# Optimization experiments

Measured on AMD Instinct MI355X. Metric: run time of the kernel, lower is better.

Reference implementation:

```python
import jax, jax.numpy as jnp
import numpy as np

EMBED = 512
HEADS = 8
HEAD_DIM = EMBED // HEADS
WINDOW = 256
HALF = WINDOW // 2
B, S = 2, 2048


def setup_inputs() -> dict:
    key = jax.random.key(0)
    kv, kk, kq, kw = jax.random.split(key, 4)
    return {
        "values": jax.random.normal(kv, (B, 1, S, EMBED), dtype=jnp.float32),
        "keys": jax.random.normal(kk, (B, 1, S, EMBED), dtype=jnp.float32),
        "query": jax.random.normal(kq, (B, 1, S, EMBED), dtype=jnp.float32),
        "mask": jnp.ones((B, 1, 1, S), dtype=jnp.int32),
        "fc_w": jax.random.normal(kw, (EMBED, EMBED), dtype=jnp.float32) * (1.0 / np.sqrt(EMBED)),
        "fc_b": jnp.zeros((EMBED,), dtype=jnp.float32),
    }


def reference(values, keys, query, mask, fc_w, fc_b):
    b = query.shape[0]
    s = values.shape[2]
    v = values.reshape(b, s, HEADS, HEAD_DIM)
    k = keys.reshape(b, s, HEADS, HEAD_DIM)
    q = query.reshape(b, s, HEADS, HEAD_DIM)
    scale = jnp.float32(EMBED ** 0.5)

    # global token: query 0 attends to all keys
    gq = q[:, 0:1]  # (b,1,h,d)
    ge = jnp.einsum('bqhd,bkhd->bhqk', gq, k)
    ga = jax.nn.softmax(ge / scale, axis=3)
    gout = jnp.einsum('bhqk,bkhd->bqhd', ga, v)  # (b,1,h,d)

    # sliding-window queries (positions 1..s-1, band centered at local index i)
    wq = q[:, 1:]  # (b, s-1, h, d)
    qw = s - 1
    e = jnp.einsum('bqhd,bkhd->bhqk', wq, k)  # (b,h,qw,s)
    i = jnp.arange(qw)[:, None]
    j = jnp.arange(s)[None, :]
    band = (j >= i - HALF) & (j <= i + HALF)  # (qw, s)
    # faithful to original: out-of-band energies are ZERO (not -inf)
    e = jnp.where(band[None, None], e, jnp.float32(0.0))
    e = jnp.where(mask == 0, jnp.float32(-1e20), e)
    a = jax.nn.softmax(e / scale, axis=3)
    lout = jnp.einsum('bhqk,bkhd->bqhd', a, v)  # (b,qw,h,d)

    out = jnp.concatenate([gout, lout], axis=1).reshape(b, s, HEADS * HEAD_DIM)
    return out @ fc_w.T + fc_b
```

## Files before the change

kernel.cpp:

```cpp
#include <hip/hip_runtime.h>
#include <math.h>

#define EMBED 512
#define HEADS 8
#define HDIM 64
#define SLEN 2048
#define BATCH 2
#define HALFW 128
#define NCHUNK 32
#define INV_SCALE 0.044194173824159216f

typedef short bf16x8 __attribute__((ext_vector_type(8)));
typedef short s16x4  __attribute__((ext_vector_type(4)));
typedef float f32x4  __attribute__((ext_vector_type(4)));

#define MFMA16(a, b, c) __builtin_amdgcn_mfma_f32_16x16x32_bf16(a, b, c, 0, 0, 0)

__device__ __forceinline__ short f2bf(float x) {
    union { float f; unsigned u; } v; v.f = x;
    unsigned r = v.u + 0x7FFFu + ((v.u >> 16) & 1u);
    return (short)(r >> 16);
}

__device__ __forceinline__ int lidx(int row, int seg) {
    return (((seg << 6) + (row ^ seg)) << 3);
}

__device__ __forceinline__ void gll16(const short* g, short* l) {
    __builtin_amdgcn_global_load_lds(
        (const __attribute__((address_space(1))) unsigned int*)g,
        (__attribute__((address_space(3))) unsigned int*)l, 16, 0, 0);
}

__device__ __forceinline__ void stage_chunk(const short* s0, const short* s1,
                                            short* d0, short* d1, int t) {
    int off = t * 8;
    int wb  = (t >> 6) * 512;
    gll16(s0 + off,        d0 + wb);
    gll16(s0 + 2048 + off, d0 + 2048 + wb);
    gll16(s1 + off,        d1 + wb);
    gll16(s1 + 2048 + off, d1 + 2048 + wb);
}

__device__ __forceinline__ void stage_tile(const short* s, short* d, int t) {
    int off = t * 8;
    int wb  = (t >> 6) * 512;
    gll16(s + off,        d + wb);
    gll16(s + 2048 + off, d + 2048 + wb);
}

__global__ __launch_bounds__(256) void prepass(
    const float* __restrict__ q, const float* __restrict__ k,
    const float* __restrict__ v, const int* __restrict__ mask,
    const float* __restrict__ fcw,
    short* __restrict__ Kbf, short* __restrict__ Vbf, short* __restrict__ Wbf,
    float* __restrict__ gnum_part, float* __restrict__ gden_part,
    float* __restrict__ vsum_part, float* __restrict__ nval_part) {
    int d = blockIdx.x;
    int x = d & 7, i = d >> 3;
    int hb8 = x * 2 + (i >= 68);
    int ii  = (i >= 68) ? (i - 68) : i;
    int h = hb8 & 7, b = hb8 >> 3;
    int t = threadIdx.x, w = t >> 6, l = t & 63;

    if (ii >= 64) {
        int widx = hb8 * 4 + (ii - 64);
        int nb = widx >> 3, kt = widx & 7;
        size_t base = (size_t)(nb * 8 + kt) * 4096;
        #pragma unroll
        for (int p = 0; p < 4; ++p) {
            int idx = p * 256 + t, row = idx >> 4, kg = idx & 15;
            float4 f = *(const float4*)(fcw + (size_t)(nb * 64 + row) * EMBED + kt * 64 + kg * 4);
            s16x4 o;
            o[0] = f2bf(f.x); o[1] = f2bf(f.y); o[2] = f2bf(f.z); o[3] = f2bf(f.w);
            *(s16x4*)&Wbf[base + lidx(row, kg >> 1) + (kg & 1) * 4] = o;
        }
        return;
    }

    int ch  = ii;
    int c   = ch >> 1;
    int rof = (ch & 1) * 32;
    int j0  = ch * 32;

    __shared__ float q0s[HDIM];
    __shared__ float wls[32];
    __shared__ int   m_s[32];
    __shared__ float vbuf[32][68];
    __shared__ float red[4][HDIM];
    __shared__ float redv[4][HDIM];

    if (t < 64) q0s[t] = q[(size_t)b * SLEN * EMBED + h * HDIM + t];
    else if (t < 96) m_s[t - 64] = mask[b * SLEN + j0 + (t - 64)];
    __syncthreads();

    size_t fragbase = ((size_t)(b * HEADS + h) * NCHUNK + c) * 4096;

    #pragma unroll
    for (int p = 0; p < 2; ++p) {
        int idx = p * 256 + t, row = idx >> 4, kg = idx & 15;
        float4 f = *(const float4*)(k + ((size_t)b * SLEN + j0 + row) * EMBED + h * HDIM + kg * 4);
        float dot = q0s[kg*4+0]*f.x + q0s[kg*4+1]*f.y + q0s[kg*4+2]*f.z + q0s[kg*4+3]*f.w;
        dot += __shfl_xor(dot, 1, 64);
        dot += __shfl_xor(dot, 2, 64);
        dot += __shfl_xor(dot, 4, 64);
        dot += __shfl_xor(dot, 8, 64);
        if ((t & 15) == 0) wls[row] = __expf(dot * INV_SCALE);
        if (!m_s[row]) f = make_float4(0.f, 0.f, 0.f, 0.f);
        s16x4 o;
        o[0] = f2bf(f.x); o[1] = f2bf(f.y); o[2] = f2bf(f.z); o[3] = f2bf(f.w);
        *(s16x4*)&Kbf[fragbase + lidx(rof + row, kg >> 1) + (kg & 1) * 4] = o;
    }

    #pragma unroll
    for (int p = 0; p < 2; ++p) {
        int idx = p * 256 + t, row = idx >> 4, kg = idx & 15;
        float4 f = *(const float4*)(v + ((size_t)b * SLEN + j0 + row) * EMBED + h * HDIM + kg * 4);
        *(float4*)&vbuf[row][kg * 4] = f;
    }
    __syncthreads();

    float num = 0.f, vs = 0.f;
    #pragma unroll
    for (int jj = 0; jj < 8; ++jj) {
        int jl = w * 8 + jj;
        float vv = vbuf[jl][l];
        num += wls[jl] * vv;
        if (m_s[jl]) vs += vv;
    }
    red[w][l] = num;
    redv[w][l] = vs;

    {
        int jseg = (ch & 1) * 4 + w;
        bf16x8 o;
        #pragma unroll
        for (int e = 0; e < 8; ++e) o[e] = f2bf(vbuf[w * 8 + e][l]);
        *(bf16x8*)&Vbf[fragbase + lidx(l, jseg)] = o;
    }
    __syncthreads();

    if (w == 0) {
        gnum_part[((size_t)(b * HEADS + h) * 64 + ch) * HDIM + l] =
            red[0][l] + red[1][l] + red[2][l] + red[3][l];
        vsum_part[((size_t)b * 64 + ch) * EMBED + h * HDIM + l] =
            redv[0][l] + redv[1][l] + redv[2][l] + redv[3][l];
    } else if (w == 1) {
        float s = (l < 32) ? wls[l] : 0.f;
        #pragma unroll
        for (int off = 32; off > 0; off >>= 1) s += __shfl_xor(s, off, 64);
        if (l == 0) gden_part[(size_t)(b * HEADS + h) * 64 + ch] = s;
    } else if (w == 2 && h == 0) {
        float cc = (l < 32 && m_s[l]) ? 1.f : 0.f;
        #pragma unroll
        for (int off = 32; off > 0; off >>= 1) cc += __shfl_xor(cc, off, 64);
        if (l == 0) nval_part[b * 64 + ch] = cc;
    }
}

__global__ __launch_bounds__(256) void windowed_attn_v9(
    const float* __restrict__ q, const float* __restrict__ k,
    const float* __restrict__ v, const int* __restrict__ mask,
    const short* __restrict__ Kbf, const short* __restrict__ Vbf,
    const float* __restrict__ gnum_part, const float* __restrict__ gden_part,
    const float* __restrict__ vsum_part, const float* __restrict__ nval_part,
    short* __restrict__ Abf) {
    int dsp = blockIdx.x;
    int wid = (dsp & 7) * 64 + (dsp >> 3);
    int tile = wid & 31, h = (wid >> 5) & 7, b = wid >> 8;
    int r0 = tile * 64;
    int t = threadIdx.x, w = t >> 6, l = t & 63;
    int lg = l >> 4, lr = l & 15;

    __shared__ __align__(16) short k_s[4][4096];
    __shared__ __align__(16) short v_s[4][4096];
    __shared__ __align__(16) short wT_s[4][16][72];
    __shared__ float rsum[64];
    __shared__ float vred[4][64];
    __shared__ float gred[4][64];
    __shared__ float nv_s, gd_s;

    size_t hb = (size_t)(b * HEADS + h) * NCHUNK;
    int bh = b * HEADS + h;

    int c0 = tile - 2; if (c0 < 0) c0 = 0;
    int c1 = tile + 2; if (c1 > NCHUNK - 1) c1 = NCHUNK - 1;

    stage_chunk(Kbf + (hb + c0) * 4096, Vbf + (hb + c0) * 4096,
                &k_s[0][0], &v_s[0][0], t);

    const float* qrow = q + ((size_t)b * SLEN + r0 + w * 16 + lr) * EMBED + h * HDIM;
    float4 a0 = *(const float4*)(qrow + lg * 8);
    float4 a1 = *(const float4*)(qrow + lg * 8 + 4);
    float4 a2 = *(const float4*)(qrow + 32 + lg * 8);
    float4 a3 = *(const float4*)(qrow + 32 + lg * 8 + 4);
    bf16x8 qb0, qb1;
    qb0[0] = f2bf(a0.x); qb0[1] = f2bf(a0.y); qb0[2] = f2bf(a0.z); qb0[3] = f2bf(a0.w);
    qb0[4] = f2bf(a1.x); qb0[5] = f2bf(a1.y); qb0[6] = f2bf(a1.z); qb0[7] = f2bf(a1.w);
    qb1[0] = f2bf(a2.x); qb1[1] = f2bf(a2.y); qb1[2] = f2bf(a2.z); qb1[3] = f2bf(a2.w);
    qb1[4] = f2bf(a3.x); qb1[5] = f2bf(a3.y); qb1[6] = f2bf(a3.z); qb1[7] = f2bf(a3.w);

    {
        float vp = 0.f;
        #pragma unroll
        for (int cc = 0; cc < 16; ++cc)
            vp += vsum_part[((size_t)b * 64 + w * 16 + cc) * EMBED + h * HDIM + l];
        vred[w][l] = vp;
        if (w == 0) {
            float nvv = nval_part[b * 64 + l];
            #pragma unroll
            for (int off = 32; off > 0; off >>= 1) nvv += __shfl_xor(nvv, off, 64);
            if (l == 0) nv_s = nvv;
        }
        if (tile == 0) {
            float gp = 0.f;
            #pragma unroll
            for (int cc = 0; cc < 16; ++cc)
                gp += gnum_part[((size_t)bh * 64 + w * 16 + cc) * HDIM + l];
            gred[w][l] = gp;
            if (w == 1) {
                float gdd = gden_part[(size_t)bh * 64 + l];
                #pragma unroll
                for (int off = 32; off > 0; off >>= 1) gdd += __shfl_xor(gdd, off, 64);
                if (l == 0) gd_s = gdd;
            }
        }
    }

    stage_chunk(Kbf + (hb + c0 + 1) * 4096, Vbf + (hb + c0 + 1) * 4096,
                &k_s[1][0], &v_s[1][0], t);
    stage_chunk(Kbf + (hb + c0 + 2) * 4096, Vbf + (hb + c0 + 2) * 4096,
                &k_s[2][0], &v_s[2][0], t);

    int center = r0 + w * 16 + lr - 1;
    int lo = center - HALFW, hi = center + HALFW;

    f32x4 pv[4];
    #pragma unroll
    for (int dt = 0; dt < 4; ++dt) pv[dt] = (f32x4){0.f, 0.f, 0.f, 0.f};
    float dacc = 0.f;

    int bi = 0;
    for (int c = c0; c <= c1; ++c) {
        int rem = c1 - c;
        if (rem >= 2)      { asm volatile("s_waitcnt vmcnt(8)" ::: "memory"); }
        else if (rem == 1) { asm volatile("s_waitcnt vmcnt(4)" ::: "memory"); }
        else               { asm volatile("s_waitcnt vmcnt(0)" ::: "memory"); }
        __syncthreads();

        int jc = c * 64;
        #pragma unroll
        for (int jt = 0; jt < 4; ++jt) {
            bf16x8 ka0 = *(const bf16x8*)&k_s[bi][lidx(jt * 16 + lr, lg)];
            bf16x8 ka1 = *(const bf16x8*)&k_s[bi][lidx(jt * 16 + lr, 4 + lg)];
            f32x4 sT = (f32x4){0.f, 0.f, 0.f, 0.f};
            sT = MFMA16(ka0, qb0, sT);
            sT = MFMA16(ka1, qb1, sT);
            int jbase = jc + jt * 16 + lg * 4;
            s16x4 wq;
            #pragma unroll
            for (int r = 0; r < 4; ++r) {
                int j = jbase + r;
                float wgt = (j >= lo && j <= hi) ? (__expf(sT[r] * INV_SCALE) - 1.f) : 0.f;
                dacc += wgt;
                wq[r] = f2bf(wgt);
            }
            *(s16x4*)&wT_s[w][lr][jt * 16 + lg * 4] = wq;
        }

        bf16x8 wa0 = *(const bf16x8*)&wT_s[w][lr][lg * 8];
        bf16x8 wa1 = *(const bf16x8*)&wT_s[w][lr][32 + lg * 8];
        #pragma unroll
        for (int dt = 0; dt < 4; ++dt) {
            bf16x8 va0 = *(const bf16x8*)&v_s[bi][lidx(dt * 16 + lr, lg)];
            bf16x8 va1 = *(const bf16x8*)&v_s[bi][lidx(dt * 16 + lr, 4 + lg)];
            pv[dt] = MFMA16(wa0, va0, pv[dt]);
            pv[dt] = MFMA16(wa1, va1, pv[dt]);
        }

        if (c + 3 <= c1) {
            int bn = (bi + 3) & 3;
            stage_chunk(Kbf + (hb + c + 3) * 4096, Vbf + (hb + c + 3) * 4096,
                        &k_s[bn][0], &v_s[bn][0], t);
        }
        bi = (bi + 1) & 3;
    }

    float wfix = 0.f;
    int jx = r0 - 129;
    if (w == 0 && jx >= 0) {
        float qv = q[((size_t)b * SLEN + r0) * EMBED + h * HDIM + l];
        float kv = k[((size_t)b * SLEN + jx) * EMBED + h * HDIM + l];
        float dd = qv * kv;
        #pragma unroll
        for (int off = 32; off > 0; off >>= 1) dd += __shfl_xor(dd, off, 64);
        if (mask[b * SLEN + jx] != 0) wfix = __expf(dd * INV_SCALE) - 1.f;
        if (lg == 0) {
            #pragma unroll
            for (int dt = 0; dt < 4; ++dt)
                pv[dt][0] += wfix * v[((size_t)b * SLEN + jx) * EMBED + h * HDIM + dt * 16 + lr];
        }
    }

    dacc += __shfl_xor(dacc, 16, 64);
    dacc += __shfl_xor(dacc, 32, 64);
    if (lg == 0) rsum[w * 16 + lr] = dacc + ((w == 0 && lr == 0) ? wfix : 0.f);
    __syncthreads();

    float nv = nv_s;
    float invden[4];
    #pragma unroll
    for (int r = 0; r < 4; ++r)
        invden[r] = 1.f / (nv + rsum[w * 16 + lg * 4 + r]);

    short* Atile = Abf + ((size_t)(b * NCHUNK + tile) * 8 + h) * 4096;
    #pragma unroll
    for (int dt = 0; dt < 4; ++dt) {
        int d = dt * 16 + lr;
        float vs = vred[0][d] + vred[1][d] + vred[2][d] + vred[3][d];
        #pragma unroll
        for (int r = 0; r < 4; ++r) {
            int row_local = w * 16 + lg * 4 + r;
            float o;
            if (tile == 0 && row_local == 0)
                o = (gred[0][d] + gred[1][d] + gred[2][d] + gred[3][d]) / gd_s;
            else
                o = (pv[dt][r] + vs) * invden[r];
            Atile[lidx(row_local, d >> 3) + (d & 7)] = f2bf(o);
        }
    }
}

__global__ __launch_bounds__(256) void fc_gemm_v5(
    const short* __restrict__ Abf, const short* __restrict__ Wbf,
    const float* __restrict__ bias, float* __restrict__ C) {
    int bm = blockIdx.x;
    int nb = blockIdx.y;
    int t = threadIdx.x, w = t >> 6, l = t & 63;
    int lg = l >> 4, lr = l & 15;
    int wr = w >> 1, wc = w & 1;

    __shared__ __align__(16) short a_s[8][4096];
    __shared__ __align__(16) short w_s[2][4096];

    stage_tile(Abf + (size_t)(bm * 8 + 0) * 4096, &a_s[0][0], t);
    stage_tile(Wbf + (size_t)(nb * 8 + 0) * 4096, &w_s[0][0], t);
    stage_tile(Wbf + (size_t)(nb * 8 + 1) * 4096, &w_s[1][0], t);
    #pragma unroll
    for (int kt = 1; kt < 8; ++kt)
        stage_tile(Abf + (size_t)(bm * 8 + kt) * 4096, &a_s[kt][0], t);

    f32x4 acc[2][2];
    #pragma unroll
    for (int mt = 0; mt < 2; ++mt)
        #pragma unroll
        for (int nt = 0; nt < 2; ++nt) acc[mt][nt] = (f32x4){0.f, 0.f, 0.f, 0.f};

    for (int kt = 0; kt < 8; ++kt) {
        if (kt == 0)      { asm volatile("s_waitcnt vmcnt(16)" ::: "memory"); }
        else if (kt == 1) { asm volatile("s_waitcnt vmcnt(14)" ::: "memory"); }
        else if (kt < 7)  { asm volatile("s_waitcnt vmcnt(2)"  ::: "memory"); }
        else              { asm volatile("s_waitcnt vmcnt(0)"  ::: "memory"); }
        __syncthreads();

        bf16x8 af[2][2], bf_[2][2];
        #pragma unroll
        for (int mt = 0; mt < 2; ++mt) {
            af[mt][0] = *(const bf16x8*)&a_s[kt][lidx(wr * 32 + mt * 16 + lr, lg)];
            af[mt][1] = *(const bf16x8*)&a_s[kt][lidx(wr * 32 + mt * 16 + lr, 4 + lg)];
        }
        int wbuf = kt & 1;
        #pragma unroll
        for (int nt = 0; nt < 2; ++nt) {
            bf_[nt][0] = *(const bf16x8*)&w_s[wbuf][lidx(wc * 32 + nt * 16 + lr, lg)];
            bf_[nt][1] = *(const bf16x8*)&w_s[wbuf][lidx(wc * 32 + nt * 16 + lr, 4 + lg)];
        }
        #pragma unroll
        for (int mt = 0; mt < 2; ++mt)
            #pragma unroll
            for (int nt = 0; nt < 2; ++nt) {
                acc[mt][nt] = MFMA16(af[mt][0], bf_[nt][0], acc[mt][nt]);
                acc[mt][nt] = MFMA16(af[mt][1], bf_[nt][1], acc[mt][nt]);
            }

        __syncthreads();
        if (kt + 2 <= 7)
            stage_tile(Wbf + (size_t)(nb * 8 + kt + 2) * 4096, &w_s[wbuf][0], t);
    }

    #pragma unroll
    for (int mt = 0; mt < 2; ++mt)
        #pragma unroll
        for (int nt = 0; nt < 2; ++nt) {
            int n = nb * 64 + wc * 32 + nt * 16 + lr;
            float bb = bias[n];
            #pragma unroll
            for (int reg = 0; reg < 4; ++reg) {
                int m = bm * 64 + wr * 32 + mt * 16 + lg * 4 + reg;
                C[(size_t)m * 512 + n] = acc[mt][nt][reg] + bb;
            }
        }
}

extern "C" void kernel_launch(void* const* d_in, const int* in_sizes, int n_in,
                              void* d_out, int out_size, void* d_ws, size_t ws_size,
                              hipStream_t stream) {
    const float* values = (const float*)d_in[0];
    const float* keys   = (const float*)d_in[1];
    const float* query  = (const float*)d_in[2];
    const int*   maskp  = (const int*)d_in[3];
    const float* fc_w   = (const float*)d_in[4];
    const float* fc_b   = (const float*)d_in[5];
    float* out = (float*)d_out;

    short* Abf = (short*)d_ws;
    short* Wbf = Abf + (size_t)BATCH * SLEN * EMBED;
    short* Kbf = Wbf + (size_t)EMBED * EMBED;
    short* Vbf = Kbf + (size_t)BATCH * HEADS * NCHUNK * 4096;
    float* vsum_part = (float*)(Vbf + (size_t)BATCH * HEADS * NCHUNK * 4096);
    float* gnum_part = vsum_part + (size_t)BATCH * 64 * EMBED;
    float* gden_part = gnum_part + (size_t)BATCH * HEADS * 64 * HDIM;
    float* nval_part = gden_part + (size_t)BATCH * HEADS * 64;

    prepass<<<dim3(1088), 256, 0, stream>>>(
        query, keys, values, maskp, fc_w, Kbf, Vbf, Wbf,
        gnum_part, gden_part, vsum_part, nval_part);
    windowed_attn_v9<<<dim3(512), 256, 0, stream>>>(
        query, keys, values, maskp, Kbf, Vbf,
        gnum_part, gden_part, vsum_part, nval_part, Abf);
    fc_gemm_v5<<<dim3(64, 8), 256, 0, stream>>>(
        Abf, Wbf, fc_b, out);
}
```

Baseline: 30.91 us.

## Fuse windowed attention and FC GEMM via per-tile atomic readiness counters

Merges the windowed-attention kernel and the FC GEMM into one launch. Each block computes its head's attention tile, then bumps a per-row-tile counter and spins until all 8 heads for that tile are written, then runs the GEMM for output column block h. Shared memory is unioned between the two phases. This removes one kernel launch and the gap between kernels, but adds inter-block spin-waiting. That wait relies on all 8 cooperating blocks being co-resident, and every block now waits for its slowest sibling.

```diff
diff --git a/kernel.cpp b/kernel.cpp
--- a/kernel.cpp
+++ b/kernel.cpp
@@ -55,8 +55,11 @@
     const float* __restrict__ fcw,
     short* __restrict__ Kbf, short* __restrict__ Vbf, short* __restrict__ Wbf,
     float* __restrict__ gnum_part, float* __restrict__ gden_part,
-    float* __restrict__ vsum_part, float* __restrict__ nval_part) {
+    float* __restrict__ vsum_part, float* __restrict__ nval_part,
+    int* __restrict__ ready) {
     int d = blockIdx.x;
+    if (d < 64 && threadIdx.x == 0) ready[d] = 0;
+
     int x = d & 7, i = d >> 3;
     int hb8 = x * 2 + (i >= 68);
     int ii  = (i >= 68) ? (i - 68) : i;
@@ -158,13 +161,30 @@
     }
 }
 
-__global__ __launch_bounds__(256) void windowed_attn_v9(
+struct WinS {
+    short k_s[4][4096];
+    short v_s[4][4096];
+    short wT_s[4][16][72];
+    float rsum[64];
+    float vred[4][64];
+    float gred[4][64];
+    float nv, gd;
+};
+struct FcS {
+    short a_s[8][4096];
+    short w_s[2][4096];
+};
+
+__global__ __launch_bounds__(256, 2) void windowed_fc_fused(
     const float* __restrict__ q, const float* __restrict__ k,
     const float* __restrict__ v, const int* __restrict__ mask,
     const short* __restrict__ Kbf, const short* __restrict__ Vbf,
+    const short* __restrict__ Wbf, const float* __restrict__ bias,
     const float* __restrict__ gnum_part, const float* __restrict__ gden_part,
     const float* __restrict__ vsum_part, const float* __restrict__ nval_part,
-    short* __restrict__ Abf) {
+    short* __restrict__ Abf, int* __restrict__ ready,
+    float* __restrict__ out) {
+    __shared__ __align__(16) char smem[sizeof(FcS)];
     int dsp = blockIdx.x;
     int wid = (dsp & 7) * 64 + (dsp >> 3);
     int tile = wid & 31, h = (wid >> 5) & 7, b = wid >> 8;
@@ -172,234 +192,233 @@
     int t = threadIdx.x, w = t >> 6, l = t & 63;
     int lg = l >> 4, lr = l & 15;
 
-    __shared__ __align__(16) short k_s[4][4096];
-    __shared__ __align__(16) short v_s[4][4096];
-    __shared__ __align__(16) short wT_s[4][16][72];
-    __shared__ float rsum[64];
-    __shared__ float vred[4][64];
-    __shared__ float gred[4][64];
-    __shared__ float nv_s, gd_s;
-
-    size_t hb = (size_t)(b * HEADS + h) * NCHUNK;
-    int bh = b * HEADS + h;
-
-    int c0 = tile - 2; if (c0 < 0) c0 = 0;
-    int c1 = tile + 2; if (c1 > NCHUNK - 1) c1 = NCHUNK - 1;
-
-    stage_chunk(Kbf + (hb + c0) * 4096, Vbf + (hb + c0) * 4096,
-                &k_s[0][0], &v_s[0][0], t);
-
-    const float* qrow = q + ((size_t)b * SLEN + r0 + w * 16 + lr) * EMBED + h * HDIM;
-    float4 a0 = *(const float4*)(qrow + lg * 8);
-    float4 a1 = *(const float4*)(qrow + lg * 8 + 4);
-    float4 a2 = *(const float4*)(qrow + 32 + lg * 8);
-    float4 a3 = *(const float4*)(qrow + 32 + lg * 8 + 4);
-    bf16x8 qb0, qb1;
-    qb0[0] = f2bf(a0.x); qb0[1] = f2bf(a0.y); qb0[2] = f2bf(a0.z); qb0[3] = f2bf(a0.w);
-    qb0[4] = f2bf(a1.x); qb0[5] = f2bf(a1.y); qb0[6] = f2bf(a1.z); qb0[7] = f2bf(a1.w);
-    qb1[0] = f2bf(a2.x); qb1[1] = f2bf(a2.y); qb1[2] = f2bf(a2.z); qb1[3] = f2bf(a2.w);
-    qb1[4] = f2bf(a3.x); qb1[5] = f2bf(a3.y); qb1[6] = f2bf(a3.z); qb1[7] = f2bf(a3.w);
-
     {
-        float vp = 0.f;
-        #pragma unroll
-        for (int cc = 0; cc < 16; ++cc)
-            vp += vsum_part[((size_t)b * 64 + w * 16 + cc) * EMBED + h * HDIM + l];
-        vred[w][l] = vp;
-        if (w == 0) {
-            float nvv = nval_part[b * 64 + l];
-            #pragma unroll
-            for (int off = 32; off > 0; off >>= 1) nvv += __shfl_xor(nvv, off, 64);
-            if (l == 0) nv_s = nvv;
-        }
-        if (tile == 0) {
-            float gp = 0.f;
+        WinS& S = *reinterpret_cast<WinS*>(smem);
+        size_t hb = (size_t)(b * HEADS + h) * NCHUNK;
+        int bh = b * HEADS + h;
+
+        int c0 = tile - 2; if (c0 < 0) c0 = 0;
+        int c1 = tile + 2; if (c1 > NCHUNK - 1) c1 = NCHUNK - 1;
+
+        stage_chunk(Kbf + (hb + c0) * 4096, Vbf + (hb + c0) * 4096,
+                    &S.k_s[0][0], &S.v_s[0][0], t);
+
+        const float* qrow = q + ((size_t)b * SLEN + r0 + w * 16 + lr) * EMBED + h * HDIM;
+        float4 a0 = *(const float4*)(qrow + lg * 8);
+        float4 a1 = *(const float4*)(qrow + lg * 8 + 4);
+        float4 a2 = *(const float4*)(qrow + 32 + lg * 8);
+        float4 a3 = *(const float4*)(qrow + 32 + lg * 8 + 4);
+        bf16x8 qb0, qb1;
+        qb0[0] = f2bf(a0.x); qb0[1] = f2bf(a0.y); qb0[2] = f2bf(a0.z); qb0[3] = f2bf(a0.w);
+        qb0[4] = f2bf(a1.x); qb0[5] = f2bf(a1.y); qb0[6] = f2bf(a1.z); qb0[7] = f2bf(a1.w);
+        qb1[0] = f2bf(a2.x); qb1[1] = f2bf(a2.y); qb1[2] = f2bf(a2.z); qb1[3] = f2bf(a2.w);
+        qb1[4] = f2bf(a3.x); qb1[5] = f2bf(a3.y); qb1[6] = f2bf(a3.z); qb1[7] = f2bf(a3.w);
+
+        {
+            float vp = 0.f;
             #pragma unroll
             for (int cc = 0; cc < 16; ++cc)
-                gp += gnum_part[((size_t)bh * 64 + w * 16 + cc) * HDIM + l];
-            gred[w][l] = gp;
-            if (w == 1) {
-                float gdd = gden_part[(size_t)bh * 64 + l];
-                #pragma unroll
-                for (int off = 32; off > 0; off >>= 1) gdd += __shfl_xor(gdd, off, 64);
-                if (l == 0) gd_s = gdd;
-            }
-        }
-    }
-
-    stage_chunk(Kbf + (hb + c0 + 1) * 4096, Vbf + (hb + c0 + 1) * 4096,
-                &k_s[1][0], &v_s[1][0], t);
-    stage_chunk(Kbf + (hb + c0 + 2) * 4096, Vbf + (hb + c0 + 2) * 4096,
-                &k_s[2][0], &v_s[2][0], t);
-
-    int center = r0 + w * 16 + lr - 1;
-    int lo = center - HALFW, hi = center + HALFW;
-
-    f32x4 pv[4];
-    #pragma unroll
-    for (int dt = 0; dt < 4; ++dt) pv[dt] = (f32x4){0.f, 0.f, 0.f, 0.f};
-    float dacc = 0.f;
-
-    int bi = 0;
-    for (int c = c0; c <= c1; ++c) {
-        int rem = c1 - c;
-        if (rem >= 2)      { asm volatile("s_waitcnt vmcnt(8)" ::: "memory"); }
-        else if (rem == 1) { asm volatile("s_waitcnt vmcnt(4)" ::: "memory"); }
-        else               { asm volatile("s_waitcnt vmcnt(0)" ::: "memory"); }
+                vp += vsum_part[((size_t)b * 64 + w * 16 + cc) * EMBED + h * HDIM + l];
+            S.vred[w][l] = vp;
+            if (w == 0) {
+                float nvv = nval_part[b * 64 + l];
+                #pragma unroll
+                for (int off = 32; off > 0; off >>= 1) nvv += __shfl_xor(nvv, off, 64);
+                if (l == 0) S.nv = nvv;
+            }
+            if (tile == 0) {
+                float gp = 0.f;
+                #pragma unroll
+                for (int cc = 0; cc < 16; ++cc)
+                    gp += gnum_part[((size_t)bh * 64 + w * 16 + cc) * HDIM + l];
+                S.gred[w][l] = gp;
+                if (w == 1) {
+                    float gdd = gden_part[(size_t)bh * 64 + l];
+                    #pragma unroll
+                    for (int off = 32; off > 0; off >>= 1) gdd += __shfl_xor(gdd, off, 64);
+                    if (l == 0) S.gd = gdd;
+                }
+            }
+        }
+
+        stage_chunk(Kbf + (hb + c0 + 1) * 4096, Vbf + (hb + c0 + 1) * 4096,
+                    &S.k_s[1][0], &S.v_s[1][0], t);
+        stage_chunk(Kbf + (hb + c0 + 2) * 4096, Vbf + (hb + c0 + 2) * 4096,
+                    &S.k_s[2][0], &S.v_s[2][0], t);
+
+        int center = r0 + w * 16 + lr - 1;
+        int lo = center - HALFW, hi = center + HALFW;
+
+        f32x4 pv[4];
+        #pragma unroll
+        for (int dt = 0; dt < 4; ++dt) pv[dt] = (f32x4){0.f, 0.f, 0.f, 0.f};
+        float dacc = 0.f;
+
+        int bi = 0;
+        for (int c = c0; c <= c1; ++c) {
+            int rem = c1 - c;
+            if (rem >= 2)      { asm volatile("s_waitcnt vmcnt(8)" ::: "memory"); }
+            else if (rem == 1) { asm volatile("s_waitcnt vmcnt(4)" ::: "memory"); }
+            else               { asm volatile("s_waitcnt vmcnt(0)" ::: "memory"); }
+            __syncthreads();
+
+            int jc = c * 64;
+            #pragma unroll
+            for (int jt = 0; jt < 4; ++jt) {
+                bf16x8 ka0 = *(const bf16x8*)&S.k_s[bi][lidx(jt * 16 + lr, lg)];
+                bf16x8 ka1 = *(const bf16x8*)&S.k_s[bi][lidx(jt * 16 + lr, 4 + lg)];
+                f32x4 sT = (f32x4){0.f, 0.f, 0.f, 0.f};
+                sT = MFMA16(ka0, qb0, sT);
+                sT = MFMA16(ka1, qb1, sT);
+                int jbase = jc + jt * 16 + lg * 4;
+                s16x4 wq;
+                #pragma unroll
+                for (int r = 0; r < 4; ++r) {
+                    int j = jbase + r;
+                    float wgt = (j >= lo && j <= hi) ? (__expf(sT[r] * INV_SCALE) - 1.f) : 0.f;
+                    dacc += wgt;
+                    wq[r] = f2bf(wgt);
+                }
+                *(s16x4*)&S.wT_s[w][lr][jt * 16 + lg * 4] = wq;
+            }
+
+            bf16x8 wa0 = *(const bf16x8*)&S.wT_s[w][lr][lg * 8];
+            bf16x8 wa1 = *(const bf16x8*)&S.wT_s[w][lr][32 + lg * 8];
+            #pragma unroll
+            for (int dt = 0; dt < 4; ++dt) {
+                bf16x8 va0 = *(const bf16x8*)&S.v_s[bi][lidx(dt * 16 + lr, lg)];
+                bf16x8 va1 = *(const bf16x8*)&S.v_s[bi][lidx(dt * 16 + lr, 4 + lg)];
+                pv[dt] = MFMA16(wa0, va0, pv[dt]);
+                pv[dt] = MFMA16(wa1, va1, pv[dt]);
+            }
+
+            if (c + 3 <= c1) {
+                int bn = (bi + 3) & 3;
+                stage_chunk(Kbf + (hb + c + 3) * 4096, Vbf + (hb + c + 3) * 4096,
+                            &S.k_s[bn][0], &S.v_s[bn][0], t);
+            }
+            bi = (bi + 1) & 3;
+        }
+
+        float wfix = 0.f;
+        int jx = r0 - 129;
+        if (w == 0 && jx >= 0) {
+            float qv = q[((size_t)b * SLEN + r0) * EMBED + h * HDIM + l];
+            float kv = k[((size_t)b * SLEN + jx) * EMBED + h * HDIM + l];
+            float dd = qv * kv;
+            #pragma unroll
+            for (int off = 32; off > 0; off >>= 1) dd += __shfl_xor(dd, off, 64);
+            if (mask[b * SLEN + jx] != 0) wfix = __expf(dd * INV_SCALE) - 1.f;
+            if (lg == 0) {
+                #pragma unroll
+                for (int dt = 0; dt < 4; ++dt)
+                    pv[dt][0] += wfix * v[((size_t)b * SLEN + jx) * EMBED + h * HDIM + dt * 16 + lr];
+            }
+        }
+
+        dacc += __shfl_xor(dacc, 16, 64);
+        dacc += __shfl_xor(dacc, 32, 64);
+        if (lg == 0) S.rsum[w * 16 + lr] = dacc + ((w == 0 && lr == 0) ? wfix : 0.f);
         __syncthreads();
 
-        int jc = c * 64;
-        #pragma unroll
-        for (int jt = 0; jt < 4; ++jt) {
-            bf16x8 ka0 = *(const bf16x8*)&k_s[bi][lidx(jt * 16 + lr, lg)];
-            bf16x8 ka1 = *(const bf16x8*)&k_s[bi][lidx(jt * 16 + lr, 4 + lg)];
-            f32x4 sT = (f32x4){0.f, 0.f, 0.f, 0.f};
-            sT = MFMA16(ka0, qb0, sT);
-            sT = MFMA16(ka1, qb1, sT);
-            int jbase = jc + jt * 16 + lg * 4;
-            s16x4 wq;
+        float nv = S.nv;
+        float invden[4];
+        #pragma unroll
+        for (int r = 0; r < 4; ++r)
+            invden[r] = 1.f / (nv + S.rsum[w * 16 + lg * 4 + r]);
+
+        short* Atile = Abf + ((size_t)(b * NCHUNK + tile) * 8 + h) * 4096;
+        #pragma unroll
+        for (int dt = 0; dt < 4; ++dt) {
+            int d = dt * 16 + lr;
+            float vs = S.vred[0][d] + S.vred[1][d] + S.vred[2][d] + S.vred[3][d];
             #pragma unroll
             for (int r = 0; r < 4; ++r) {
-                int j = jbase + r;
-                float wgt = (j >= lo && j <= hi) ? (__expf(sT[r] * INV_SCALE) - 1.f) : 0.f;
-                dacc += wgt;
-                wq[r] = f2bf(wgt);
-            }
-            *(s16x4*)&wT_s[w][lr][jt * 16 + lg * 4] = wq;
-        }
-
-        bf16x8 wa0 = *(const bf16x8*)&wT_s[w][lr][lg * 8];
-        bf16x8 wa1 = *(const bf16x8*)&wT_s[w][lr][32 + lg * 8];
-        #pragma unroll
-        for (int dt = 0; dt < 4; ++dt) {
-            bf16x8 va0 = *(const bf16x8*)&v_s[bi][lidx(dt * 16 + lr, lg)];
-            bf16x8 va1 = *(const bf16x8*)&v_s[bi][lidx(dt * 16 + lr, 4 + lg)];
-            pv[dt] = MFMA16(wa0, va0, pv[dt]);
-            pv[dt] = MFMA16(wa1, va1, pv[dt]);
-        }
-
-        if (c + 3 <= c1) {
-            int bn = (bi + 3) & 3;
-            stage_chunk(Kbf + (hb + c + 3) * 4096, Vbf + (hb + c + 3) * 4096,
-                        &k_s[bn][0], &v_s[bn][0], t);
-        }
-        bi = (bi + 1) & 3;
-    }
-
-    float wfix = 0.f;
-    int jx = r0 - 129;
-    if (w == 0 && jx >= 0) {
-        float qv = q[((size_t)b * SLEN + r0) * EMBED + h * HDIM + l];
-        float kv = k[((size_t)b * SLEN + jx) * EMBED + h * HDIM + l];
-        float dd = qv * kv;
-        #pragma unroll
-        for (int off = 32; off > 0; off >>= 1) dd += __shfl_xor(dd, off, 64);
-        if (mask[b * SLEN + jx] != 0) wfix = __expf(dd * INV_SCALE) - 1.f;
-        if (lg == 0) {
-            #pragma unroll
-            for (int dt = 0; dt < 4; ++dt)
-                pv[dt][0] += wfix * v[((size_t)b * SLEN + jx) * EMBED + h * HDIM + dt * 16 + lr];
-        }
-    }
-
-    dacc += __shfl_xor(dacc, 16, 64);
-    dacc += __shfl_xor(dacc, 32, 64);
-    if (lg == 0) rsum[w * 16 + lr] = dacc + ((w == 0 && lr == 0) ? wfix : 0.f);
+                int row_local = w * 16 + lg * 4 + r;
+                float o;
+                if (tile == 0 && row_local == 0)
+                    o = (S.gred[0][d] + S.gred[1][d] + S.gred[2][d] + S.gred[3][d]) / S.gd;
+                else
+                    o = (pv[dt][r] + vs) * invden[r];
+                Atile[lidx(row_local, d >> 3) + (d & 7)] = f2bf(o);
+            }
+        }
+    }
+
+    int bm = b * NCHUNK + tile;
+    int nb = h;
+    asm volatile("s_waitcnt vmcnt(0)" ::: "memory");
     __syncthreads();
-
-    float nv = nv_s;
-    float invden[4];
-    #pragma unroll
-    for (int r = 0; r < 4; ++r)
-        invden[r] = 1.f / (nv + rsum[w * 16 + lg * 4 + r]);
-
-    short* Atile = Abf + ((size_t)(b * NCHUNK + tile) * 8 + h) * 4096;
-    #pragma unroll
-    for (int dt = 0; dt < 4; ++dt) {
-        int d = dt * 16 + lr;
-        float vs = vred[0][d] + vred[1][d] + vred[2][d] + vred[3][d];
-        #pragma unroll
-        for (int r = 0; r < 4; ++r) {
-            int row_local = w * 16 + lg * 4 + r;
-            float o;
-            if (tile == 0 && row_local == 0)
-                o = (gred[0][d] + gred[1][d] + gred[2][d] + gred[3][d]) / gd_s;
-            else
-                o = (pv[dt][r] + vs) * invden[r];
-            Atile[lidx(row_local, d >> 3) + (d & 7)] = f2bf(o);
-        }
-    }
-}
-
-__global__ __launch_bounds__(256) void fc_gemm_v5(
-    const short* __restrict__ Abf, const short* __restrict__ Wbf,
-    const float* __restrict__ bias, float* __restrict__ C) {
-    int bm = blockIdx.x;
-    int nb = blockIdx.y;
-    int t = threadIdx.x, w = t >> 6, l = t & 63;
-    int lg = l >> 4, lr = l & 15;
-    int wr = w >> 1, wc = w & 1;
-
-    __shared__ __align__(16) short a_s[8][4096];
-    __shared__ __align__(16) short w_s[2][4096];
-
-    stage_tile(Abf + (size_t)(bm * 8 + 0) * 4096, &a_s[0][0], t);
-    stage_tile(Wbf + (size_t)(nb * 8 + 0) * 4096, &w_s[0][0], t);
-    stage_tile(Wbf + (size_t)(nb * 8 + 1) * 4096, &w_s[1][0], t);
-    #pragma unroll
-    for (int kt = 1; kt < 8; ++kt)
-        stage_tile(Abf + (size_t)(bm * 8 + kt) * 4096, &a_s[kt][0], t);
-
-    f32x4 acc[2][2];
-    #pragma unroll
-    for (int mt = 0; mt < 2; ++mt)
-        #pragma unroll
-        for (int nt = 0; nt < 2; ++nt) acc[mt][nt] = (f32x4){0.f, 0.f, 0.f, 0.f};
-
-    for (int kt = 0; kt < 8; ++kt) {
-        if (kt == 0)      { asm volatile("s_waitcnt vmcnt(16)" ::: "memory"); }
-        else if (kt == 1) { asm volatile("s_waitcnt vmcnt(14)" ::: "memory"); }
-        else if (kt < 7)  { asm volatile("s_waitcnt vmcnt(2)"  ::: "memory"); }
-        else              { asm volatile("s_waitcnt vmcnt(0)"  ::: "memory"); }
-        __syncthreads();
-
-        bf16x8 af[2][2], bf_[2][2];
-        #pragma unroll
-        for (int mt = 0; mt < 2; ++mt) {
-            af[mt][0] = *(const bf16x8*)&a_s[kt][lidx(wr * 32 + mt * 16 + lr, lg)];
-            af[mt][1] = *(const bf16x8*)&a_s[kt][lidx(wr * 32 + mt * 16 + lr, 4 + lg)];
-        }
-        int wbuf = kt & 1;
-        #pragma unroll
-        for (int nt = 0; nt < 2; ++nt) {
-            bf_[nt][0] = *(const bf16x8*)&w_s[wbuf][lidx(wc * 32 + nt * 16 + lr, lg)];
-            bf_[nt][1] = *(const bf16x8*)&w_s[wbuf][lidx(wc * 32 + nt * 16 + lr, 4 + lg)];
-        }
+    if (t == 0) {
+        __builtin_amdgcn_fence(__ATOMIC_RELEASE, "agent");
+        __hip_atomic_fetch_add(&ready[bm], 1, __ATOMIC_RELAXED, __HIP_MEMORY_SCOPE_AGENT);
+        while (__hip_atomic_load(&ready[bm], __ATOMIC_RELAXED, __HIP_MEMORY_SCOPE_AGENT) < 8) {}
+        __builtin_amdgcn_fence(__ATOMIC_ACQUIRE, "agent");
+    }
+    __syncthreads();
+
+    {
+        FcS& S = *reinterpret_cast<FcS*>(smem);
+        int wr = w >> 1, wc = w & 1;
+
+        stage_tile(Abf + (size_t)(bm * 8 + 0) * 4096, &S.a_s[0][0], t);
+        stage_tile(Wbf + (size_t)(nb * 8 + 0) * 4096, &S.w_s[0][0], t);
+        stage_tile(Wbf + (size_t)(nb * 8 + 1) * 4096, &S.w_s[1][0], t);
+        #pragma unroll
+        for (int kt = 1; kt < 8; ++kt)
+            stage_tile(Abf + (size_t)(bm * 8 + kt) * 4096, &S.a_s[kt][0], t);
+
+        f32x4 acc[2][2];
         #pragma unroll
         for (int mt = 0; mt < 2; ++mt)
             #pragma unroll
+            for (int nt = 0; nt < 2; ++nt) acc[mt][nt] = (f32x4){0.f, 0.f, 0.f, 0.f};
+
+        for (int kt = 0; kt < 8; ++kt) {
+            if (kt == 0)      { asm volatile("s_waitcnt vmcnt(16)" ::: "memory"); }
+            else if (kt == 1) { asm volatile("s_waitcnt vmcnt(14)" ::: "memory"); }
+            else if (kt < 7)  { asm volatile("s_waitcnt vmcnt(2)"  ::: "memory"); }
+            else              { asm volatile("s_waitcnt vmcnt(0)"  ::: "memory"); }
+            __syncthreads();
+
+            bf16x8 af[2][2], bf_[2][2];
+            #pragma unroll
+            for (int mt = 0; mt < 2; ++mt) {
+                af[mt][0] = *(const bf16x8*)&S.a_s[kt][lidx(wr * 32 + mt * 16 + lr, lg)];
+                af[mt][1] = *(const bf16x8*)&S.a_s[kt][lidx(wr * 32 + mt * 16 + lr, 4 + lg)];
+            }
+            int wbuf = kt & 1;
+            #pragma unroll
             for (int nt = 0; nt < 2; ++nt) {
-                acc[mt][nt] = MFMA16(af[mt][0], bf_[nt][0], acc[mt][nt]);
-                acc[mt][nt] = MFMA16(af[mt][1], bf_[nt][1], acc[mt][nt]);
-            }
-
-        __syncthreads();
-        if (kt + 2 <= 7)
-            stage_tile(Wbf + (size_t)(nb * 8 + kt + 2) * 4096, &w_s[wbuf][0], t);
-    }
-
-    #pragma unroll
-    for (int mt = 0; mt < 2; ++mt)
-        #pragma unroll
-        for (int nt = 0; nt < 2; ++nt) {
-            int n = nb * 64 + wc * 32 + nt * 16 + lr;
-            float bb = bias[n];
-            #pragma unroll
-            for (int reg = 0; reg < 4; ++reg) {
-                int m = bm * 64 + wr * 32 + mt * 16 + lg * 4 + reg;
-                C[(size_t)m * 512 + n] = acc[mt][nt][reg] + bb;
-            }
-        }
+                bf_[nt][0] = *(const bf16x8*)&S.w_s[wbuf][lidx(wc * 32 + nt * 16 + lr, lg)];
+                bf_[nt][1] = *(const bf16x8*)&S.w_s[wbuf][lidx(wc * 32 + nt * 16 + lr, 4 + lg)];
+            }
+            #pragma unroll
+            for (int mt = 0; mt < 2; ++mt)
+                #pragma unroll
+                for (int nt = 0; nt < 2; ++nt) {
+                    acc[mt][nt] = MFMA16(af[mt][0], bf_[nt][0], acc[mt][nt]);
+                    acc[mt][nt] = MFMA16(af[mt][1], bf_[nt][1], acc[mt][nt]);
+                }
+
+            __syncthreads();
+            if (kt + 2 <= 7)
+                stage_tile(Wbf + (size_t)(nb * 8 + kt + 2) * 4096, &S.w_s[wbuf][0], t);
+        }
+
+        #pragma unroll
+        for (int mt = 0; mt < 2; ++mt)
+            #pragma unroll
+            for (int nt = 0; nt < 2; ++nt) {
+                int n = nb * 64 + wc * 32 + nt * 16 + lr;
+                float bb = bias[n];
+                #pragma unroll
+                for (int reg = 0; reg < 4; ++reg) {
+                    int m = bm * 64 + wr * 32 + mt * 16 + lg * 4 + reg;
+                    out[(size_t)m * 512 + n] = acc[mt][nt][reg] + bb;
+                }
+            }
+    }
 }
 
 extern "C" void kernel_launch(void* const* d_in, const int* in_sizes, int n_in,
@@ -421,13 +440,12 @@
     float* gnum_part = vsum_part + (size_t)BATCH * 64 * EMBED;
     float* gden_part = gnum_part + (size_t)BATCH * HEADS * 64 * HDIM;
     float* nval_part = gden_part + (size_t)BATCH * HEADS * 64;
+    int*   ready     = (int*)(nval_part + BATCH * 64);
 
     prepass<<<dim3(1088), 256, 0, stream>>>(
         query, keys, values, maskp, fc_w, Kbf, Vbf, Wbf,
-        gnum_part, gden_part, vsum_part, nval_part);
-    windowed_attn_v9<<<dim3(512), 256, 0, stream>>>(
-        query, keys, values, maskp, Kbf, Vbf,
-        gnum_part, gden_part, vsum_part, nval_part, Abf);
-    fc_gemm_v5<<<dim3(64, 8), 256, 0, stream>>>(
-        Abf, Wbf, fc_b, out);
-}
+        gnum_part, gden_part, vsum_part, nval_part, ready);
+    windowed_fc_fused<<<dim3(512), 256, 0, stream>>>(
+        query, keys, values, maskp, Kbf, Vbf, Wbf, fc_b,
+        gnum_part, gden_part, vsum_part, nval_part, Abf, ready, out);
+}
```

Result: slower. 54.67 us (+76.9%).
